# Performance work log

Hardware: AMD Instinct MI355X
Metric: run time of the kernel (lower is better)

The kernel has to match this reference:

```python
import jax, jax.numpy as jnp
import numpy as np

N_ATOMS = 50000
IN_DIM = 128
HID = 256
N_ELEM = 4
N_IMG = 500
NNZ = 2_000_000
ELEMENTS = jnp.array([1, 6, 8, 29], dtype=jnp.int64)


def setup_inputs() -> dict:
    key = jax.random.key(0)
    ks = jax.random.split(key, 14)
    fingerprints = jax.random.normal(ks[0], (N_ATOMS, IN_DIM), dtype=jnp.float32)
    # atomic numbers drawn from the supported element set
    elem_idx = jax.random.randint(ks[1], (N_ATOMS,), 0, N_ELEM)
    atomic_numbers = ELEMENTS[elem_idx]
    image_idx = jnp.sort(jax.random.randint(ks[2], (N_ATOMS,), 0, N_IMG))
    # sparse fprimes (COO): [N_ATOMS*IN_DIM, 3*N_ATOMS]
    fprime_rows = jax.random.randint(ks[3], (NNZ,), 0, N_ATOMS * IN_DIM)
    fprime_cols = jax.random.randint(ks[4], (NNZ,), 0, 3 * N_ATOMS)
    fprime_vals = jax.random.normal(ks[5], (NNZ,), dtype=jnp.float32) * 0.1
    # per-element MLP params, stacked over the element axis (torch Linear-style init)
    s0, s1 = 1.0 / np.sqrt(IN_DIM), 1.0 / np.sqrt(HID)
    W0 = jax.random.uniform(ks[6], (N_ELEM, IN_DIM, HID), jnp.float32, -s0, s0)
    b0 = jax.random.uniform(ks[7], (N_ELEM, HID), jnp.float32, -s0, s0)
    W1 = jax.random.uniform(ks[8], (N_ELEM, HID, HID), jnp.float32, -s1, s1)
    b1 = jax.random.uniform(ks[9], (N_ELEM, HID), jnp.float32, -s1, s1)
    W2 = jax.random.uniform(ks[10], (N_ELEM, HID, 1), jnp.float32, -s1, s1)
    b2 = jax.random.uniform(ks[11], (N_ELEM, 1), jnp.float32, -s1, s1)
    return {"fingerprints": fingerprints, "atomic_numbers": atomic_numbers,
            "image_idx": image_idx, "fprime_rows": fprime_rows,
            "fprime_cols": fprime_cols, "fprime_vals": fprime_vals,
            "W0": W0, "b0": b0, "W1": W1, "b1": b1, "W2": W2, "b2": b2}


def _per_atom_energy(fp, atomic_numbers, W0, b0, W1, b1, W2, b2):
    # Run every element-specific MLP over ALL atoms (as the torch module does),
    # then mask by the one-hot element membership and sum over elements.
    h = jnp.tanh(jnp.einsum('nd,edh->enh', fp, W0) + b0[:, None, :])   # [E,N,H]
    h = jnp.tanh(jnp.einsum('enh,ehk->enk', h, W1) + b1[:, None, :])   # [E,N,H]
    out = jnp.einsum('enh,eho->eno', h, W2) + b2[:, None, :]           # [E,N,1]
    mask = (atomic_numbers[None, :] == ELEMENTS[:, None]).astype(fp.dtype)  # [E,N]
    return jnp.sum(mask * out[..., 0], axis=0)                          # [N]


def reference(fingerprints, atomic_numbers, image_idx, fprime_rows,
              fprime_cols, fprime_vals, W0, b0, W1, b1, W2, b2):
    o = _per_atom_energy(fingerprints, atomic_numbers, W0, b0, W1, b1, W2, b2)
    energy = jax.ops.segment_sum(o, image_idx, num_segments=N_IMG)  # [N_IMG]
    # dE/dfp for forces (sum over images == sum over atoms of o)
    g = jax.grad(lambda fp: jnp.sum(
        _per_atom_energy(fp, atomic_numbers, W0, b0, W1, b1, W2, b2)))(fingerprints)
    g_flat = g.reshape(-1)  # [N*D]
    # forces = -fprimes^T @ g_flat, fprimes in COO form
    forces = -jax.ops.segment_sum(fprime_vals * g_flat[fprime_rows],
                                  fprime_cols, num_segments=3 * N_ATOMS)
    return energy, forces.reshape(N_ATOMS, 3)
```

## Files before the change

### kernel.cpp

```cpp
#include <hip/hip_runtime.h>
#include <math.h>

#define N_ATOMS 50000
#define IN_DIM 128
#define HID 256
#define N_ELEM 4
#define N_IMG 500
#define NNZ 2000000

#define CBINS 293
#define CW 512
#define BCAP 8192
#define OCAP 4096
#define PCH 2560
#define NBP ((NNZ + PCH - 1) / PCH)
#define BKB ((N_ATOMS + 255) / 256)

typedef __attribute__((ext_vector_type(8))) short bf16x8;
typedef __attribute__((ext_vector_type(4))) float f32x4;
typedef __attribute__((ext_vector_type(4))) int   i32x4;
typedef __attribute__((ext_vector_type(4))) float fv4;

__device__ __forceinline__ int elem_of(int z) {
    return (z == 1) ? 0 : (z == 6) ? 1 : (z == 8) ? 2 : 3;
}

__device__ __forceinline__ unsigned short f2bf(float f) {
    unsigned u = __float_as_uint(f);
    u += 0x7fffu + ((u >> 16) & 1u);
    return (unsigned short)(u >> 16);
}
__device__ __forceinline__ float bf2f(unsigned short u) {
    return __uint_as_float(((unsigned)u) << 16);
}
__device__ __forceinline__ float tanh_fast(float x) {
    float e = __expf(2.f * x);
    return (e - 1.f) / (e + 1.f);
}

__global__ __launch_bounds__(256) void prep_weights(
    const float* __restrict__ W0, const float* __restrict__ W1,
    unsigned short* __restrict__ W0s1,
    unsigned short* __restrict__ W1s2,
    unsigned short* __restrict__ W1s3,
    unsigned short* __restrict__ W0s4,
    int* __restrict__ counts, int* __restrict__ gcur, int* __restrict__ ocur) {
    if (blockIdx.x == 0) {
        if (threadIdx.x < N_ELEM) counts[threadIdx.x] = 0;
        for (int i = threadIdx.x; i < CBINS; i += 256) gcur[i] = 0;
        if (threadIdx.x == 0) ocur[0] = 0;
    }
    const int T = blockIdx.x * 256 + threadIdx.x;

    if (T < 32768) {
        const int e = T >> 13, fid = T & 8191;
        const int blkv = fid >> 6, lane = fid & 63;
        const int k0 = ((blkv & 7) << 5) | ((lane >> 4) << 3);
        const int n  = ((blkv >> 3) << 4) | (lane & 15);
        const float* src = W1 + e * 65536 + n;
        bf16x8 vv;
#pragma unroll
        for (int j = 0; j < 8; ++j) vv[j] = (short)f2bf(src[(k0 + j) * 256]);
        *(bf16x8*)(W1s2 + (e << 16) + (fid << 3)) = vv;
    } else if (T < 65536) {
        const int u = T - 32768, e = u >> 13, fid = u & 8191;
        const int blkv = fid >> 6, lane = fid & 63;
        const int k  = ((blkv >> 3) << 4) | (lane & 15);
        const int n0 = ((blkv & 7) << 5) | ((lane >> 4) << 3);
        const float* src = W1 + e * 65536 + k * 256 + n0;
        float4 a = *(const float4*)src;
        float4 b = *(const float4*)(src + 4);
        bf16x8 vv;
        vv[0] = (short)f2bf(a.x); vv[1] = (short)f2bf(a.y);
        vv[2] = (short)f2bf(a.z); vv[3] = (short)f2bf(a.w);
        vv[4] = (short)f2bf(b.x); vv[5] = (short)f2bf(b.y);
        vv[6] = (short)f2bf(b.z); vv[7] = (short)f2bf(b.w);
        *(bf16x8*)(W1s3 + (e << 16) + (fid << 3)) = vv;
    } else if (T < 81920) {
        const int u = T - 65536, e = u >> 12, fid = u & 4095;
        const int blkv = fid >> 6, lane = fid & 63;
        const int k0 = ((blkv & 3) << 5) | ((lane >> 4) << 3);
        const int n  = ((blkv >> 2) << 4) | (lane & 15);
        const float* src = W0 + e * 32768 + n;
        bf16x8 vv;
#pragma unroll
        for (int j = 0; j < 8; ++j) vv[j] = (short)f2bf(src[(k0 + j) * 256]);
        *(bf16x8*)(W0s1 + e * 32768 + (fid << 3)) = vv;
    } else if (T < 98304) {
        const int u = T - 81920, e = u >> 12, fid = u & 4095;
        const int blkv = fid >> 6, lane = fid & 63;
        const int k  = ((blkv >> 3) << 4) | (lane & 15);
        const int n0 = ((blkv & 7) << 5) | ((lane >> 4) << 3);
        const float* src = W0 + e * 32768 + k * 256 + n0;
        float4 a = *(const float4*)src;
        float4 b = *(const float4*)(src + 4);
        bf16x8 vv;
        vv[0] = (short)f2bf(a.x); vv[1] = (short)f2bf(a.y);
        vv[2] = (short)f2bf(a.z); vv[3] = (short)f2bf(a.w);
        vv[4] = (short)f2bf(b.x); vv[5] = (short)f2bf(b.y);
        vv[6] = (short)f2bf(b.z); vv[7] = (short)f2bf(b.w);
        *(bf16x8*)(W0s4 + e * 32768 + (fid << 3)) = vv;
    }
}

__global__ __launch_bounds__(256) void bucket_atoms(
    const int* __restrict__ Z, int* __restrict__ counts,
    int* __restrict__ lists, float* __restrict__ F) {
    __shared__ int lcnt[N_ELEM], lbase[N_ELEM];
    const int tid = threadIdx.x;
    const int bb = blockIdx.x;
    for (int idx = bb * 256 + tid; idx < 3 * N_ATOMS; idx += BKB * 256)
        F[idx] = 0.f;
    const int i = bb * 256 + tid;
    if (tid < N_ELEM) lcnt[tid] = 0;
    __syncthreads();
    int e = -1, pos = 0;
    if (i < N_ATOMS) {
        e = elem_of(Z[i]);
        pos = atomicAdd(&lcnt[e], 1);
    }
    __syncthreads();
    if (tid < N_ELEM) lbase[tid] = atomicAdd(&counts[tid], lcnt[tid]);
    __syncthreads();
    if (i < N_ATOMS) lists[e * N_ATOMS + lbase[e] + pos] = i;
}

#define TILES_PER_E 512
#define CH 1280
__global__ __launch_bounds__(256, 4) void mega_mlp_bin(
    const float* __restrict__ fp,
    const unsigned short* __restrict__ W0s1,
    const unsigned short* __restrict__ W1s2,
    const unsigned short* __restrict__ W1s3,
    const unsigned short* __restrict__ W0s4,
    const float* __restrict__ b0, const float* __restrict__ b1,
    const float* __restrict__ W2, const float* __restrict__ b2,
    float* __restrict__ o_atom,
    unsigned short* __restrict__ Gb,
    const int* __restrict__ counts, const int* __restrict__ lists,
    const int* __restrict__ rows, const int* __restrict__ cols,
    const float* __restrict__ vals,
    unsigned* __restrict__ packB, float* __restrict__ valsB,
    int* __restrict__ gcur,
    int* __restrict__ ovfR, int* __restrict__ ovfC, float* __restrict__ ovfV,
    int* __restrict__ ocur) {

    __shared__ __align__(16) char smem[40960];
    const int tid = threadIdx.x;
    const int bid = blockIdx.x;

    if (bid < NBP) {
        int*   Lr    = (int*)smem;
        int*   Lc    = (int*)(smem + 10240);
        float* Lv    = (float*)(smem + 20480);
        int*   hist  = (int*)(smem + 30720);
        int*   pref  = (int*)(smem + 31892);
        int*   curs  = (int*)(smem + 33064);
        int*   gbase = (int*)(smem + 34236);

        const int base = bid * PCH;
        const int lim = (base + PCH <= NNZ) ? PCH : (NNZ - base);

        for (int i = tid; i < CBINS; i += 256) hist[i] = 0;
        __syncthreads();

        i32x4 r[3], c[3];
        fv4   v[3];
        int nvalid[3];
#pragma unroll
        for (int j = 0; j < 3; ++j) {
            const int li = tid * 4 + 1024 * j;
            const int i0 = base + li;
            int nv = lim - li;
            nvalid[j] = nv > 4 ? 4 : (nv < 0 ? 0 : nv);
            if (nvalid[j] == 4) {
                r[j] = __builtin_nontemporal_load((const i32x4*)(rows + i0));
                c[j] = __builtin_nontemporal_load((const i32x4*)(cols + i0));
                v[j] = __builtin_nontemporal_load((const fv4*)(vals + i0));
            } else {
                for (int e2 = 0; e2 < nvalid[j]; ++e2) {
                    r[j][e2] = rows[i0 + e2]; c[j][e2] = cols[i0 + e2];
                    v[j][e2] = vals[i0 + e2];
                }
            }
#pragma unroll
            for (int e2 = 0; e2 < 4; ++e2)
                if (e2 < nvalid[j]) atomicAdd(&hist[c[j][e2] >> 9], 1);
        }
        __syncthreads();

        if (tid == 0) {
            int s = 0;
            for (int b = 0; b < CBINS; ++b) { pref[b] = s; s += hist[b]; }
        }
        __syncthreads();
        for (int b = tid; b < CBINS; b += 256) {
            gbase[b] = atomicAdd(&gcur[b], hist[b]);
            curs[b] = pref[b];
        }
        __syncthreads();

#pragma unroll
        for (int j = 0; j < 3; ++j)
#pragma unroll
            for (int e2 = 0; e2 < 4; ++e2)
                if (e2 < nvalid[j]) {
                    int b = c[j][e2] >> 9;
                    int p = atomicAdd(&curs[b], 1);
                    Lr[p] = r[j][e2]; Lc[p] = c[j][e2]; Lv[p] = v[j][e2];
                }
        __syncthreads();

#pragma unroll
        for (int j = 0; j < 10; ++j) {
            const int p = tid + 256 * j;
            if (p >= lim) break;
            const int col = Lc[p];
            const int b = col >> 9;
            const int g = gbase[b] + (p - pref[b]);
            if (g < BCAP) {
                packB[b * BCAP + g] = ((unsigned)(col & 511) << 23) | (unsigned)Lr[p];
                valsB[b * BCAP + g] = Lv[p];
            } else {
                int od = atomicAdd(ocur, 1);
                if (od < OCAP) { ovfR[od] = Lr[p]; ovfC[od] = col; ovfV[od] = Lv[p]; }
            }
        }
        return;
    }

    const int fid = bid - NBP;
    const int xcd = fid & 7;
    const int e = xcd & 3;
    const int tile = (fid >> 3) * 2 + (xcd >> 2);
    const int cnt = counts[e];
    const int m0 = tile * 32;
    if (m0 >= cnt) return;
    const int* list = lists + e * N_ATOMS;

    short* tH = (short*)smem;
    short* tD = (short*)(smem + 20480);

    const int lane = tid & 63;
    const int wv = tid >> 6;
    const int lr = lane & 15;
    const int lq = lane >> 4;

    const unsigned short* B1 = W0s1 + (size_t)e * HID * IN_DIM;
    const unsigned short* B2 = W1s2 + (size_t)e * HID * HID;
    const unsigned short* B3 = W1s3 + (size_t)e * HID * HID;
    const unsigned short* B4 = W0s4 + (size_t)e * IN_DIM * HID;

    f32x4 acc[2][4];
#define ZERO_ACC()                                                        \
    _Pragma("unroll") for (int mt = 0; mt < 2; ++mt)                      \
        _Pragma("unroll") for (int nt = 0; nt < 4; ++nt)                  \
            _Pragma("unroll") for (int j = 0; j < 4; ++j) acc[mt][nt][j] = 0.f;

    {
        bf16x8 bb0[4];
#pragma unroll
        for (int nt = 0; nt < 4; ++nt)
            bb0[nt] = *(const bf16x8*)(B1 +
                ((size_t)(((wv * 4 + nt) * 4 + 0) * 64 + lane) << 3));

#pragma unroll
        for (int p = 0; p < 4; ++p) {
            const int row = p * 8 + (tid >> 5);
            const int col = (tid & 31) * 4;
            const int m = m0 + row;
            float4 a = make_float4(0.f, 0.f, 0.f, 0.f);
            if (m < cnt)
                a = *(const float4*)(fp + (size_t)list[m] * IN_DIM + col);
            short4 b;
            b.x = (short)f2bf(a.x); b.y = (short)f2bf(a.y);
            b.z = (short)f2bf(a.z); b.w = (short)f2bf(a.w);
            *(short4*)&tD[(col >> 5) * CH + row * 40 + (col & 31)] = b;
        }
        __syncthreads();

        ZERO_ACC();
        bf16x8 bb[2][4];
#pragma unroll
        for (int nt = 0; nt < 4; ++nt) bb[0][nt] = bb0[nt];
#pragma unroll
        for (int ki = 0; ki < 4; ++ki) {
            const int cur = ki & 1, nx = cur ^ 1;
            if (ki < 3) {
#pragma unroll
                for (int nt = 0; nt < 4; ++nt)
                    bb[nx][nt] = *(const bf16x8*)(B1 +
                        ((size_t)(((wv * 4 + nt) * 4 + ki + 1) * 64 + lane) << 3));
            }
            bf16x8 af[2];
#pragma unroll
            for (int mt = 0; mt < 2; ++mt)
                af[mt] = *(const bf16x8*)&tD[ki * CH + (mt * 16 + lr) * 40 + lq * 8];
#pragma unroll
            for (int mt = 0; mt < 2; ++mt)
#pragma unroll
                for (int nt = 0; nt < 4; ++nt)
                    acc[mt][nt] = __builtin_amdgcn_mfma_f32_16x16x32_bf16(
                        af[mt], bb[cur][nt], acc[mt][nt], 0, 0, 0);
        }
    }

    bf16x8 b2r[3][4];
#pragma unroll
    for (int p = 0; p < 3; ++p)
#pragma unroll
        for (int nt = 0; nt < 4; ++nt)
            b2r[p][nt] = *(const bf16x8*)(B2 +
                ((size_t)(((wv * 4 + nt) * 8 + p) * 64 + lane) << 3));

    {
        float bv[4];
#pragma unroll
        for (int nt = 0; nt < 4; ++nt)
            bv[nt] = b0[e * HID + wv * 64 + nt * 16 + lr];
#pragma unroll
        for (int mt = 0; mt < 2; ++mt)
#pragma unroll
            for (int rr = 0; rr < 4; ++rr) {
                const int row = mt * 16 + lq * 4 + rr;
#pragma unroll
                for (int nt = 0; nt < 4; ++nt) {
                    const int n = wv * 64 + nt * 16 + lr;
                    float t = tanh_fast(acc[mt][nt][rr] + bv[nt]);
                    tH[(n >> 5) * CH + row * 40 + (n & 31)] = (short)f2bf(t);
                }
            }
    }
    __syncthreads();

    ZERO_ACC();
#pragma unroll
    for (int ki = 0; ki < 8; ++ki) {
        bf16x8 af[2];
#pragma unroll
        for (int mt = 0; mt < 2; ++mt)
            af[mt] = *(const bf16x8*)&tH[ki * CH + (mt * 16 + lr) * 40 + lq * 8];
#pragma unroll
        for (int mt = 0; mt < 2; ++mt)
#pragma unroll
            for (int nt = 0; nt < 4; ++nt)
                acc[mt][nt] = __builtin_amdgcn_mfma_f32_16x16x32_bf16(
                    af[mt], b2r[ki % 3][nt], acc[mt][nt], 0, 0, 0);
        if (ki < 5) {
#pragma unroll
            for (int nt = 0; nt < 4; ++nt)
                b2r[ki % 3][nt] = *(const bf16x8*)(B2 +
                    ((size_t)(((wv * 4 + nt) * 8 + ki + 3) * 64 + lane) << 3));
        }
    }

    bf16x8 b3r[3][4];
#pragma unroll
    for (int p = 0; p < 3; ++p)
#pragma unroll
        for (int nt = 0; nt < 4; ++nt)
            b3r[p][nt] = *(const bf16x8*)(B3 +
                ((size_t)(((wv * 4 + nt) * 8 + p) * 64 + lane) << 3));

    {
        float bv[4], w2v[4];
#pragma unroll
        for (int nt = 0; nt < 4; ++nt) {
            bv[nt]  = b1[e * HID + wv * 64 + nt * 16 + lr];
            w2v[nt] = W2[e * HID + wv * 64 + nt * 16 + lr];
        }
#pragma unroll
        for (int mt = 0; mt < 2; ++mt)
#pragma unroll
            for (int rr = 0; rr < 4; ++rr) {
                const int row = mt * 16 + lq * 4 + rr;
                float osum = 0.f;
#pragma unroll
                for (int nt = 0; nt < 4; ++nt) {
                    const int n = wv * 64 + nt * 16 + lr;
                    float t = tanh_fast(acc[mt][nt][rr] + bv[nt]);
                    osum += t * w2v[nt];
                    tD[(n >> 5) * CH + row * 40 + (n & 31)] =
                        (short)f2bf(w2v[nt] * (1.f - t * t));
                }
                osum += __shfl_xor(osum, 1, 64);
                osum += __shfl_xor(osum, 2, 64);
                osum += __shfl_xor(osum, 4, 64);
                osum += __shfl_xor(osum, 8, 64);
                if (lr == 0)
                    ((float*)&tD[row * 40 + 32])[wv] = osum;
            }
    }
    __syncthreads();
    if (tid < 32) {
        int m = m0 + tid;
        if (m < cnt) {
            const float4 r4 = *(const float4*)&tD[tid * 40 + 32];
            o_atom[list[m]] = r4.x + r4.y + r4.z + r4.w + b2[e];
        }
    }

    ZERO_ACC();
#pragma unroll
    for (int ki = 0; ki < 8; ++ki) {
        bf16x8 af[2];
#pragma unroll
        for (int mt = 0; mt < 2; ++mt)
            af[mt] = *(const bf16x8*)&tD[ki * CH + (mt * 16 + lr) * 40 + lq * 8];
#pragma unroll
        for (int mt = 0; mt < 2; ++mt)
#pragma unroll
            for (int nt = 0; nt < 4; ++nt)
                acc[mt][nt] = __builtin_amdgcn_mfma_f32_16x16x32_bf16(
                    af[mt], b3r[ki % 3][nt], acc[mt][nt], 0, 0, 0);
        if (ki < 5) {
#pragma unroll
            for (int nt = 0; nt < 4; ++nt)
                b3r[ki % 3][nt] = *(const bf16x8*)(B3 +
                    ((size_t)(((wv * 4 + nt) * 8 + ki + 3) * 64 + lane) << 3));
        }
    }

    bf16x8 b4r[3][2];
#pragma unroll
    for (int p = 0; p < 3; ++p)
#pragma unroll
        for (int nt = 0; nt < 2; ++nt)
            b4r[p][nt] = *(const bf16x8*)(B4 +
                ((size_t)(((wv * 2 + nt) * 8 + p) * 64 + lane) << 3));

#pragma unroll
    for (int mt = 0; mt < 2; ++mt)
#pragma unroll
        for (int rr = 0; rr < 4; ++rr) {
            const int row = mt * 16 + lq * 4 + rr;
#pragma unroll
            for (int nt = 0; nt < 4; ++nt) {
                const int n = wv * 64 + nt * 16 + lr;
                const int a = (n >> 5) * CH + row * 40 + (n & 31);
                float h = bf2f((unsigned short)tH[a]);
                tH[a] = (short)f2bf(acc[mt][nt][rr] * (1.f - h * h));
            }
        }
    __syncthreads();

    {
        f32x4 a4[2][2];
#pragma unroll
        for (int mt = 0; mt < 2; ++mt)
#pragma unroll
            for (int nt = 0; nt < 2; ++nt)
#pragma unroll
                for (int j = 0; j < 4; ++j) a4[mt][nt][j] = 0.f;
#pragma unroll
        for (int ki = 0; ki < 8; ++ki) {
            bf16x8 af[2];
#pragma unroll
            for (int mt = 0; mt < 2; ++mt)
                af[mt] = *(const bf16x8*)&tH[ki * CH + (mt * 16 + lr) * 40 + lq * 8];
#pragma unroll
            for (int mt = 0; mt < 2; ++mt)
#pragma unroll
                for (int nt = 0; nt < 2; ++nt)
                    a4[mt][nt] = __builtin_amdgcn_mfma_f32_16x16x32_bf16(
                        af[mt], b4r[ki % 3][nt], a4[mt][nt], 0, 0, 0);
            if (ki < 5) {
#pragma unroll
                for (int nt = 0; nt < 2; ++nt)
                    b4r[ki % 3][nt] = *(const bf16x8*)(B4 +
                        ((size_t)(((wv * 2 + nt) * 8 + ki + 3) * 64 + lane) << 3));
            }
        }
#pragma unroll
        for (int mt = 0; mt < 2; ++mt)
#pragma unroll
            for (int rr = 0; rr < 4; ++rr) {
                const int row = mt * 16 + lq * 4 + rr;
#pragma unroll
                for (int nt = 0; nt < 2; ++nt) {
                    const int n = wv * 32 + nt * 16 + lr;
                    tD[(n >> 5) * CH + row * 40 + (n & 31)] =
                        (short)f2bf(a4[mt][nt][rr]);
                }
            }
    }
    __syncthreads();
#pragma unroll
    for (int t = 0; t < 2; ++t) {
        const int c = tid + 256 * t;
        const int row = c >> 4;
        const int pos = (c & 15) * 8;
        const int m = m0 + row;
        if (m < cnt) {
            bf16x8 v = *(const bf16x8*)&tD[(pos >> 5) * CH + row * 40 + (pos & 31)];
            *(bf16x8*)(Gb + (size_t)list[m] * IN_DIM + pos) = v;
        }
    }
#undef ZERO_ACC
}

__global__ __launch_bounds__(1024) void forces_consumer(
    const unsigned* __restrict__ packB, const float* __restrict__ valsB,
    const int* __restrict__ gcur,
    const unsigned short* __restrict__ g, float* __restrict__ F,
    const float* __restrict__ o_atom, const int* __restrict__ img,
    float* __restrict__ energy,
    const int* __restrict__ ovfR, const int* __restrict__ ovfC,
    const float* __restrict__ ovfV, const int* __restrict__ ocur) {

    const int blk = blockIdx.x;
    __shared__ float win[CW];

    if (blk < CBINS) {
        for (int i = threadIdx.x; i < CW; i += 1024) win[i] = 0.f;
        __syncthreads();
        const int w0 = blk << 9;
        int cnt = gcur[blk]; if (cnt > BCAP) cnt = BCAP;
        const size_t o = (size_t)blk * BCAP;
        for (int idx0 = (int)threadIdx.x * 4; idx0 < cnt; idx0 += 4096) {
            if (idx0 + 4 <= cnt) {
                i32x4 p = *(const i32x4*)((const int*)packB + o + idx0);
                fv4   v = *(const fv4*)(valsB + o + idx0);
                unsigned p0 = (unsigned)p[0], p1 = (unsigned)p[1];
                unsigned p2 = (unsigned)p[2], p3 = (unsigned)p[3];
                float g0 = bf2f(g[p0 & 0x7FFFFFu]), g1 = bf2f(g[p1 & 0x7FFFFFu]);
                float g2 = bf2f(g[p2 & 0x7FFFFFu]), g3 = bf2f(g[p3 & 0x7FFFFFu]);
                atomicAdd(&win[p0 >> 23], -v[0] * g0);
                atomicAdd(&win[p1 >> 23], -v[1] * g1);
                atomicAdd(&win[p2 >> 23], -v[2] * g2);
                atomicAdd(&win[p3 >> 23], -v[3] * g3);
            } else {
                for (int e2 = idx0; e2 < cnt; ++e2) {
                    unsigned p0 = packB[o + e2];
                    atomicAdd(&win[p0 >> 23],
                              -valsB[o + e2] * bf2f(g[p0 & 0x7FFFFFu]));
                }
            }
        }
        int ocnt = ocur[0]; if (ocnt > OCAP) ocnt = OCAP;
        for (int k2 = threadIdx.x; k2 < ocnt; k2 += 1024) {
            int c = ovfC[k2];
            if (c >= w0 && c < w0 + CW)
                atomicAdd(&win[c - w0], -ovfV[k2] * bf2f(g[ovfR[k2]]));
        }
        __syncthreads();
        for (int i = threadIdx.x; i < CW; i += 1024) {
            int c = w0 + i;
            if (c < 3 * N_ATOMS) F[c] = win[i];
        }
    }

    if (blk < N_IMG) {
        const int bb = blk;
        int lo, hi;
        {
            int l = 0, r = N_ATOMS;
            while (l < r) { int m = (l + r) >> 1; if (img[m] < bb) l = m + 1; else r = m; }
            lo = l;
        }
        {
            int l = lo, r = N_ATOMS;
            while (l < r) { int m = (l + r) >> 1; if (img[m] < bb + 1) l = m + 1; else r = m; }
            hi = l;
        }
        float s = 0.f;
        for (int i2 = lo + (int)threadIdx.x; i2 < hi; i2 += 1024) s += o_atom[i2];
#pragma unroll
        for (int off = 32; off > 0; off >>= 1) s += __shfl_down(s, off, 64);
        __shared__ float red[16];
        if ((threadIdx.x & 63) == 0) red[threadIdx.x >> 6] = s;
        __syncthreads();
        if (threadIdx.x == 0) {
            float t = 0.f;
#pragma unroll
            for (int w = 0; w < 16; ++w) t += red[w];
            energy[bb] = t;
        }
    }
}

extern "C" void kernel_launch(void* const* d_in, const int* in_sizes, int n_in,
                              void* d_out, int out_size, void* d_ws, size_t ws_size,
                              hipStream_t stream) {
    const float* fp    = (const float*)d_in[0];
    const int*   Z     = (const int*)d_in[1];
    const int*   img   = (const int*)d_in[2];
    const int*   frows = (const int*)d_in[3];
    const int*   fcols = (const int*)d_in[4];
    const float* fvals = (const float*)d_in[5];
    const float* W0    = (const float*)d_in[6];
    const float* b0    = (const float*)d_in[7];
    const float* W1    = (const float*)d_in[8];
    const float* b1    = (const float*)d_in[9];
    const float* W2    = (const float*)d_in[10];
    const float* b2    = (const float*)d_in[11];

    float* out    = (float*)d_out;
    float* energy = out;
    float* F      = out + N_IMG;

    char* ws = (char*)d_ws;
    int*   counts = (int*)ws;
    int*   lists  = (int*)(ws + 1024);
    char*  base   = ws + (1 << 20);
    unsigned short* Gb   = (unsigned short*)(base);
    float* o_atom        = (float*)(base + 13000000);
    unsigned short* W0s1 = (unsigned short*)(base + 14000000);
    unsigned short* W0s4 = W0s1 + N_ELEM * IN_DIM * HID;
    unsigned short* W1s2 = W0s4 + N_ELEM * IN_DIM * HID;
    unsigned short* W1s3 = W1s2 + N_ELEM * HID * HID;
    int*   gcur  = (int*)(base + 18000000);
    int*   ocur  = (int*)(base + 18002048);
    unsigned* packB = (unsigned*)(base + 19000000);
    float* valsB = (float*)(base + 29000000);
    int*   ovfR  = (int*)(base + 49000000);
    int*   ovfC  = (int*)(base + 49050000);
    float* ovfV  = (float*)(base + 49100000);

    prep_weights<<<384, 256, 0, stream>>>(
        W0, W1, W0s1, W1s2, W1s3, W0s4, counts, gcur, ocur);

    bucket_atoms<<<BKB, 256, 0, stream>>>(Z, counts, lists, F);

    mega_mlp_bin<<<NBP + 8 * (TILES_PER_E / 2), 256, 0, stream>>>(
        fp, W0s1, W1s2, W1s3, W0s4, b0, b1, W2, b2, o_atom, Gb, counts, lists,
        frows, fcols, fvals, packB, valsB, gcur, ovfR, ovfC, ovfV, ocur);

    forces_consumer<<<N_IMG, 1024, 0, stream>>>(
        packB, valsB, gcur, Gb, F, o_atom, img, energy,
        ovfR, ovfC, ovfV, ocur);
}
```

Baseline: 208.5 us.

## Merge prep and bucket kernels, interleave binning blocks, split force bins across blocks

Merges weight preparation and atom bucketing into a single launch and replaces the counter-zeroing done by block 0 with a memset. In the fused MLP/binning kernel, COO binning blocks are spread evenly among the MLP tile blocks rather than all running first. The force consumer now gives each column bin to two blocks that accumulate into F atomically, and energy segments get their own blocks. The aim is fewer launches, better overlap between the binning and MLP phases, and more parallelism in the consumer, at the cost of extra global atomics and a memset.

```diff
diff --git a/kernel.cpp b/kernel.cpp
--- a/kernel.cpp
+++ b/kernel.cpp
@@ -12,9 +12,13 @@
 #define CW 512
 #define BCAP 8192
 #define OCAP 4096
+#define CSPLIT 2
 #define PCH 2560
 #define NBP ((NNZ + PCH - 1) / PCH)
+#define NFB 2048
+#define TOTB (NBP + NFB)
 #define BKB ((N_ATOMS + 255) / 256)
+#define PREPB 384
 
 typedef __attribute__((ext_vector_type(8))) short bf16x8;
 typedef __attribute__((ext_vector_type(4))) float f32x4;
@@ -38,19 +42,38 @@
     return (e - 1.f) / (e + 1.f);
 }
 
-__global__ __launch_bounds__(256) void prep_weights(
+__global__ __launch_bounds__(256) void prep_and_bucket(
     const float* __restrict__ W0, const float* __restrict__ W1,
     unsigned short* __restrict__ W0s1,
     unsigned short* __restrict__ W1s2,
     unsigned short* __restrict__ W1s3,
     unsigned short* __restrict__ W0s4,
-    int* __restrict__ counts, int* __restrict__ gcur, int* __restrict__ ocur) {
-    if (blockIdx.x == 0) {
-        if (threadIdx.x < N_ELEM) counts[threadIdx.x] = 0;
-        for (int i = threadIdx.x; i < CBINS; i += 256) gcur[i] = 0;
-        if (threadIdx.x == 0) ocur[0] = 0;
-    }
-    const int T = blockIdx.x * 256 + threadIdx.x;
+    const int* __restrict__ Z, int* __restrict__ counts,
+    int* __restrict__ lists, float* __restrict__ F) {
+
+    const int tid = threadIdx.x;
+
+    if (blockIdx.x >= PREPB) {
+        __shared__ int lcnt[N_ELEM], lbase[N_ELEM];
+        const int bb = blockIdx.x - PREPB;
+        for (int idx = bb * 256 + tid; idx < 3 * N_ATOMS; idx += BKB * 256)
+            F[idx] = 0.f;
+        const int i = bb * 256 + tid;
+        if (tid < N_ELEM) lcnt[tid] = 0;
+        __syncthreads();
+        int e = -1, pos = 0;
+        if (i < N_ATOMS) {
+            e = elem_of(Z[i]);
+            pos = atomicAdd(&lcnt[e], 1);
+        }
+        __syncthreads();
+        if (tid < N_ELEM) lbase[tid] = atomicAdd(&counts[tid], lcnt[tid]);
+        __syncthreads();
+        if (i < N_ATOMS) lists[e * N_ATOMS + lbase[e] + pos] = i;
+        return;
+    }
+
+    const int T = blockIdx.x * 256 + tid;
 
     if (T < 32768) {
         const int e = T >> 13, fid = T & 8191;
@@ -103,28 +126,6 @@
     }
 }
 
-__global__ __launch_bounds__(256) void bucket_atoms(
-    const int* __restrict__ Z, int* __restrict__ counts,
-    int* __restrict__ lists, float* __restrict__ F) {
-    __shared__ int lcnt[N_ELEM], lbase[N_ELEM];
-    const int tid = threadIdx.x;
-    const int bb = blockIdx.x;
-    for (int idx = bb * 256 + tid; idx < 3 * N_ATOMS; idx += BKB * 256)
-        F[idx] = 0.f;
-    const int i = bb * 256 + tid;
-    if (tid < N_ELEM) lcnt[tid] = 0;
-    __syncthreads();
-    int e = -1, pos = 0;
-    if (i < N_ATOMS) {
-        e = elem_of(Z[i]);
-        pos = atomicAdd(&lcnt[e], 1);
-    }
-    __syncthreads();
-    if (tid < N_ELEM) lbase[tid] = atomicAdd(&counts[tid], lcnt[tid]);
-    __syncthreads();
-    if (i < N_ATOMS) lists[e * N_ATOMS + lbase[e] + pos] = i;
-}
-
 #define TILES_PER_E 512
 #define CH 1280
 __global__ __launch_bounds__(256, 4) void mega_mlp_bin(
@@ -147,9 +148,12 @@
 
     __shared__ __align__(16) char smem[40960];
     const int tid = threadIdx.x;
+
     const int bid = blockIdx.x;
-
-    if (bid < NBP) {
+    const int pA = (bid * NBP) / TOTB;
+    const int pB = ((bid + 1) * NBP) / TOTB;
+
+    if (pB > pA) {
         int*   Lr    = (int*)smem;
         int*   Lc    = (int*)(smem + 10240);
         float* Lv    = (float*)(smem + 20480);
@@ -158,7 +162,7 @@
         int*   curs  = (int*)(smem + 33064);
         int*   gbase = (int*)(smem + 34236);
 
-        const int base = bid * PCH;
+        const int base = pA * PCH;
         const int lim = (base + PCH <= NNZ) ? PCH : (NNZ - base);
 
         for (int i = tid; i < CBINS; i += 256) hist[i] = 0;
@@ -229,7 +233,7 @@
         return;
     }
 
-    const int fid = bid - NBP;
+    const int fid = bid - pB;
     const int xcd = fid & 7;
     const int e = xcd & 3;
     const int tile = (fid >> 3) * 2 + (xcd >> 2);
@@ -509,15 +513,17 @@
     const float* __restrict__ ovfV, const int* __restrict__ ocur) {
 
     const int blk = blockIdx.x;
-    __shared__ float win[CW];
-
-    if (blk < CBINS) {
+
+    if (blk < CBINS * CSPLIT) {
+        __shared__ float win[CW];
+        const int w = blk / CSPLIT, half = blk % CSPLIT;
         for (int i = threadIdx.x; i < CW; i += 1024) win[i] = 0.f;
         __syncthreads();
-        const int w0 = blk << 9;
-        int cnt = gcur[blk]; if (cnt > BCAP) cnt = BCAP;
-        const size_t o = (size_t)blk * BCAP;
-        for (int idx0 = (int)threadIdx.x * 4; idx0 < cnt; idx0 += 4096) {
+        const int w0 = w << 9;
+        int cnt = gcur[w]; if (cnt > BCAP) cnt = BCAP;
+        const size_t o = (size_t)w * BCAP;
+        for (int idx0 = (int)threadIdx.x * 4 + half * 4096; idx0 < cnt;
+             idx0 += 4096 * CSPLIT) {
             if (idx0 + 4 <= cnt) {
                 i32x4 p = *(const i32x4*)((const int*)packB + o + idx0);
                 fv4   v = *(const fv4*)(valsB + o + idx0);
@@ -537,21 +543,24 @@
                 }
             }
         }
-        int ocnt = ocur[0]; if (ocnt > OCAP) ocnt = OCAP;
-        for (int k2 = threadIdx.x; k2 < ocnt; k2 += 1024) {
-            int c = ovfC[k2];
-            if (c >= w0 && c < w0 + CW)
-                atomicAdd(&win[c - w0], -ovfV[k2] * bf2f(g[ovfR[k2]]));
+        if (half == 0) {
+            int ocnt = ocur[0]; if (ocnt > OCAP) ocnt = OCAP;
+            for (int k2 = threadIdx.x; k2 < ocnt; k2 += 1024) {
+                int c = ovfC[k2];
+                if (c >= w0 && c < w0 + CW)
+                    atomicAdd(&win[c - w0], -ovfV[k2] * bf2f(g[ovfR[k2]]));
+            }
         }
         __syncthreads();
         for (int i = threadIdx.x; i < CW; i += 1024) {
             int c = w0 + i;
-            if (c < 3 * N_ATOMS) F[c] = win[i];
-        }
-    }
-
-    if (blk < N_IMG) {
-        const int bb = blk;
+            if (c < 3 * N_ATOMS) atomicAdd(&F[c], win[i]);
+        }
+        return;
+    }
+
+    {
+        const int bb = blk - CBINS * CSPLIT;
         int lo, hi;
         {
             int l = 0, r = N_ATOMS;
@@ -573,7 +582,7 @@
         if (threadIdx.x == 0) {
             float t = 0.f;
 #pragma unroll
-            for (int w = 0; w < 16; ++w) t += red[w];
+            for (int w2 = 0; w2 < 16; ++w2) t += red[w2];
             energy[bb] = t;
         }
     }
@@ -601,7 +610,9 @@
 
     char* ws = (char*)d_ws;
     int*   counts = (int*)ws;
-    int*   lists  = (int*)(ws + 1024);
+    int*   gcur   = (int*)(ws + 32);
+    int*   ocur   = (int*)(ws + 32 + 4 * CBINS);
+    int*   lists  = (int*)(ws + 4096);
     char*  base   = ws + (1 << 20);
     unsigned short* Gb   = (unsigned short*)(base);
     float* o_atom        = (float*)(base + 13000000);
@@ -609,24 +620,22 @@
     unsigned short* W0s4 = W0s1 + N_ELEM * IN_DIM * HID;
     unsigned short* W1s2 = W0s4 + N_ELEM * IN_DIM * HID;
     unsigned short* W1s3 = W1s2 + N_ELEM * HID * HID;
-    int*   gcur  = (int*)(base + 18000000);
-    int*   ocur  = (int*)(base + 18002048);
     unsigned* packB = (unsigned*)(base + 19000000);
     float* valsB = (float*)(base + 29000000);
     int*   ovfR  = (int*)(base + 49000000);
     int*   ovfC  = (int*)(base + 49050000);
     float* ovfV  = (float*)(base + 49100000);
 
-    prep_weights<<<384, 256, 0, stream>>>(
-        W0, W1, W0s1, W1s2, W1s3, W0s4, counts, gcur, ocur);
-
-    bucket_atoms<<<BKB, 256, 0, stream>>>(Z, counts, lists, F);
-
-    mega_mlp_bin<<<NBP + 8 * (TILES_PER_E / 2), 256, 0, stream>>>(
+    hipMemsetAsync(ws, 0, 32 + 4 * CBINS + 4, stream);
+
+    prep_and_bucket<<<PREPB + BKB, 256, 0, stream>>>(
+        W0, W1, W0s1, W1s2, W1s3, W0s4, Z, counts, lists, F);
+
+    mega_mlp_bin<<<TOTB, 256, 0, stream>>>(
         fp, W0s1, W1s2, W1s3, W0s4, b0, b1, W2, b2, o_atom, Gb, counts, lists,
         frows, fcols, fvals, packB, valsB, gcur, ovfR, ovfC, ovfV, ocur);
 
-    forces_consumer<<<N_IMG, 1024, 0, stream>>>(
+    forces_consumer<<<CBINS * CSPLIT + N_IMG, 1024, 0, stream>>>(
         packB, valsB, gcur, Gb, F, o_atom, img, energy,
         ovfR, ovfC, ovfV, ocur);
 }
```

Measured after the change: 196.0 us. 1.06x faster.
